# Optimization experiments

Hardware: AMD Instinct MI355X
Metric: run time of the kernel (lower is better)

## Reference

```python
import jax, jax.numpy as jnp
import numpy as np

NUM_EXPERTS = 16
IN_FEATURES = 2048
OUT_FEATURES = 2048
RANK = 128
ALPHA = 32.0
TOKENS = 32768  # total packed tokens, multiple of NUM_EXPERTS (pad_seq_to_mult guarantees this)


def setup_inputs() -> dict:
    key = jax.random.key(0)
    k1, k2, k3 = jax.random.split(key, 3)
    x = jax.random.normal(k1, (TOKENS, IN_FEATURES), dtype=jnp.float32)
    # linear_in per-expert weights (kaiming-style random for reference)
    lora_a = jax.random.normal(k2, (NUM_EXPERTS, IN_FEATURES, RANK), dtype=jnp.float32) * (1.0 / np.sqrt(IN_FEATURES))
    # linear_out per-expert weights (LoRA convention init is zeros; random here for nontrivial check)
    lora_b = jax.random.normal(k3, (NUM_EXPERTS, RANK, OUT_FEATURES), dtype=jnp.float32) * (1.0 / np.sqrt(RANK))
    return {"x": x, "lora_a": lora_a, "lora_b": lora_b}


def reference(x, lora_a, lora_b):
    # Tokens are packed per expert with uniform counts (padding to a multiple of
    # NUM_EXPERTS is handled upstream by pad_seq_to_mult). Grouped LoRA:
    #   out_e = (x_e @ A_e) @ B_e * (alpha / rank)
    E = lora_a.shape[0]
    T, H = x.shape
    xg = x.reshape(E, T // E, H)                      # [E, Te, H]
    low = jnp.einsum('eth,ehr->etr', xg, lora_a)      # grouped GEMM 1: [E, Te, r]
    # activation = identity (adapter default)
    out = jnp.einsum('etr,ero->eto', low, lora_b)     # grouped GEMM 2: [E, Te, O]
    scale = ALPHA / RANK
    return (out * scale).reshape(T, -1)               # [T, O]
```

## Files before the change

### kernel.cpp

```cpp
#include <hip/hip_runtime.h>
#include <hip/hip_bf16.h>
#include <stdint.h>

#define NEXP   16
#define TTOK   32768
#define HIN    2048
#define RNK    128
#define OOUT   2048
#define TE     (TTOK / NEXP)
#define LORA_SCALE 0.25f

typedef __bf16 bf16_t;
typedef bf16_t bf16x8 __attribute__((ext_vector_type(8)));
typedef bf16_t bf16x4 __attribute__((ext_vector_type(4)));
typedef float  f32x4  __attribute__((ext_vector_type(4)));

__global__ void transpose_cvt_kernel(const float* __restrict__ src,
                                     bf16_t* __restrict__ dst,
                                     int Rr, int Cc)
{
    __shared__ float tile[32][33];
    const int e  = blockIdx.z;
    const int c0 = blockIdx.x * 32;
    const int r0 = blockIdx.y * 32;
    const float* s = src + (size_t)e * Rr * Cc;
    bf16_t*      d = dst + (size_t)e * Rr * Cc;
    const int tx = threadIdx.x & 31;
    const int ty = threadIdx.x >> 5;
#pragma unroll
    for (int j = 0; j < 32; j += 8)
        tile[ty + j][tx] = s[(size_t)(r0 + ty + j) * Cc + (c0 + tx)];
    __syncthreads();
#pragma unroll
    for (int j = 0; j < 32; j += 8)
        d[(size_t)(c0 + ty + j) * Rr + (r0 + tx)] = (bf16_t)tile[tx][ty + j];
}

__global__ __launch_bounds__(512, 2)
void fused_lora(const float* __restrict__ X,
                const bf16_t* __restrict__ Atw,
                const bf16_t* __restrict__ Btw,
                float* __restrict__ Out)
{
    __shared__ __align__(16) char lds[98304];

    const int tid  = threadIdx.x;
    const int blk  = blockIdx.x;
    const int m0   = blk * 128;
    const int e    = blk >> 4;

    const int wave = tid >> 6;
    const int lane = tid & 63;
    const int lm   = lane & 15;
    const int q    = lane >> 4;
    const int wr   = (wave >> 1) * 32;
    const int wc   = (wave & 1) * 64;

    const int sr  = tid >> 2;
    const int sc  = tid & 3;
    const int ssw = (sr & 7) << 4;

    const float*  xg = X   + (size_t)(m0 + sr) * HIN + sc * 16;
    const bf16_t* ag = Atw + ((size_t)e * RNK + sr) * HIN + sc * 16;

    f32x4  xa[4];
    bf16x8 ar[2];
    f32x4  acc1[2][4] = {};

    {
#pragma unroll
        for (int i = 0; i < 4; ++i) xa[i] = *(const f32x4*)(xg + i * 4);
        ar[0] = *(const bf16x8*)(ag);
        ar[1] = *(const bf16x8*)(ag + 8);
        bf16x8 c0, c1;
#pragma unroll
        for (int i = 0; i < 4; ++i) {
            c0[i] = (bf16_t)xa[0][i]; c0[4 + i] = (bf16_t)xa[1][i];
            c1[i] = (bf16_t)xa[2][i]; c1[4 + i] = (bf16_t)xa[3][i];
        }
        char* bx = lds + sr * 128;
        *(bf16x8*)(bx + ((sc * 32     ) ^ ssw)) = c0;
        *(bf16x8*)(bx + ((sc * 32 + 16) ^ ssw)) = c1;
        char* ba = lds + 32768 + sr * 128;
        *(bf16x8*)(ba + ((sc * 32     ) ^ ssw)) = ar[0];
        *(bf16x8*)(ba + ((sc * 32 + 16) ^ ssw)) = ar[1];
    }
    __syncthreads();

    for (int it = 0; it < 32; ++it) {
        const int cur = it & 1;
        if (it < 31) {
            const float*  px = xg + (it + 1) * 64;
            const bf16_t* pa = ag + (it + 1) * 64;
#pragma unroll
            for (int i = 0; i < 4; ++i) xa[i] = *(const f32x4*)(px + i * 4);
            ar[0] = *(const bf16x8*)(pa);
            ar[1] = *(const bf16x8*)(pa + 8);
        }
        const char* xb = lds + cur * 16384;
        const char* ab = lds + 32768 + cur * 16384;
#pragma unroll
        for (int ks = 0; ks < 2; ++ks) {
            bf16x8 XF[2], AF[4];
#pragma unroll
            for (int mt = 0; mt < 2; ++mt) {
                const int row = wr + mt * 16 + lm;
                XF[mt] = *(const bf16x8*)(xb + row * 128 +
                           ((ks * 64 + q * 16) ^ ((row & 7) << 4)));
            }
#pragma unroll
            for (int rt = 0; rt < 4; ++rt) {
                const int row = wc + rt * 16 + lm;
                AF[rt] = *(const bf16x8*)(ab + row * 128 +
                           ((ks * 64 + q * 16) ^ ((row & 7) << 4)));
            }
#pragma unroll
            for (int mt = 0; mt < 2; ++mt)
#pragma unroll
                for (int rt = 0; rt < 4; ++rt)
                    acc1[mt][rt] = __builtin_amdgcn_mfma_f32_16x16x32_bf16(
                        AF[rt], XF[mt], acc1[mt][rt], 0, 0, 0);
        }
        if (it < 31) {
            bf16x8 c0, c1;
#pragma unroll
            for (int i = 0; i < 4; ++i) {
                c0[i] = (bf16_t)xa[0][i]; c0[4 + i] = (bf16_t)xa[1][i];
                c1[i] = (bf16_t)xa[2][i]; c1[4 + i] = (bf16_t)xa[3][i];
            }
            char* bx = lds + (cur ^ 1) * 16384 + sr * 128;
            *(bf16x8*)(bx + ((sc * 32     ) ^ ssw)) = c0;
            *(bf16x8*)(bx + ((sc * 32 + 16) ^ ssw)) = c1;
            char* ba = lds + 32768 + (cur ^ 1) * 16384 + sr * 128;
            *(bf16x8*)(ba + ((sc * 32     ) ^ ssw)) = ar[0];
            *(bf16x8*)(ba + ((sc * 32 + 16) ^ ssw)) = ar[1];
        }
        __syncthreads();
    }

    bf16x8 br[4];
    const bf16_t* bg0 = Btw + ((size_t)e * OOUT + sr) * RNK + sc * 32;
#pragma unroll
    for (int i = 0; i < 4; ++i) br[i] = *(const bf16x8*)(bg0 + i * 8);

    char* Lbase = lds + 65536;
#pragma unroll
    for (int mt = 0; mt < 2; ++mt) {
        const int m   = wr + mt * 16 + lm;
        const int msw = (m & 7) << 4;
#pragma unroll
        for (int rt = 0; rt < 4; ++rt) {
            const int r0 = wc + rt * 16 + q * 4;
            bf16x4 v;
#pragma unroll
            for (int i = 0; i < 4; ++i) v[i] = (bf16_t)acc1[mt][rt][i];
            *(bf16x4*)(Lbase + m * 256 + ((r0 * 2) ^ msw)) = v;
        }
    }
    __syncthreads();

    bf16x8 af2[2][4];
#pragma unroll
    for (int mt = 0; mt < 2; ++mt) {
        const int m   = wr + mt * 16 + lm;
        const int msw = (m & 7) << 4;
#pragma unroll
        for (int ks = 0; ks < 4; ++ks)
            af2[mt][ks] = *(const bf16x8*)(Lbase + m * 256 +
                             ((ks * 64 + q * 16) ^ msw));
    }

    {
        char* bb = lds + sr * 256;
#pragma unroll
        for (int i = 0; i < 4; ++i)
            *(bf16x8*)(bb + ((sc * 64 + i * 16) ^ ssw)) = br[i];
    }
    __syncthreads();

    for (int c = 0; c < 16; ++c) {
        const int cur = c & 1;
        if (c < 15) {
            const bf16_t* bg = bg0 + (size_t)(c + 1) * 128 * RNK;
#pragma unroll
            for (int i = 0; i < 4; ++i) br[i] = *(const bf16x8*)(bg + i * 8);
        }
        f32x4 acc2[2][4] = {};
        const char* bb = lds + cur * 32768;
#pragma unroll
        for (int nt = 0; nt < 4; ++nt) {
            const int n   = wc + nt * 16 + lm;
            const int nsw = (n & 7) << 4;
#pragma unroll
            for (int ks = 0; ks < 4; ++ks) {
                const bf16x8 bfr = *(const bf16x8*)(bb + n * 256 +
                                      ((ks * 64 + q * 16) ^ nsw));
                acc2[0][nt] = __builtin_amdgcn_mfma_f32_16x16x32_bf16(
                    bfr, af2[0][ks], acc2[0][nt], 0, 0, 0);
                acc2[1][nt] = __builtin_amdgcn_mfma_f32_16x16x32_bf16(
                    bfr, af2[1][ks], acc2[1][nt], 0, 0, 0);
            }
        }
#pragma unroll
        for (int mt = 0; mt < 2; ++mt) {
            const int gm = m0 + wr + mt * 16 + lm;
            float* orow = Out + (size_t)gm * OOUT + c * 128 + wc + q * 4;
#pragma unroll
            for (int nt = 0; nt < 4; ++nt) {
                const f32x4 v = acc2[mt][nt] * LORA_SCALE;
                *(f32x4*)(orow + nt * 16) = v;
            }
        }
        if (c < 15) {
            char* bb2 = lds + (cur ^ 1) * 32768 + sr * 256;
#pragma unroll
            for (int i = 0; i < 4; ++i)
                *(bf16x8*)(bb2 + ((sc * 64 + i * 16) ^ ssw)) = br[i];
        }
        __syncthreads();
    }
}

extern "C" void kernel_launch(void* const* d_in, const int* in_sizes, int n_in,
                              void* d_out, int out_size, void* d_ws, size_t ws_size,
                              hipStream_t stream)
{
    const float* x  = (const float*)d_in[0];
    const float* la = (const float*)d_in[1];
    const float* lb = (const float*)d_in[2];
    float* out = (float*)d_out;

    bf16_t* At  = (bf16_t*)d_ws;
    bf16_t* Btw = At + (size_t)NEXP * RNK * HIN;

    {
        dim3 g(RNK / 32, HIN / 32, NEXP);
        transpose_cvt_kernel<<<g, 256, 0, stream>>>(la, At, HIN, RNK);
    }
    {
        dim3 g(OOUT / 32, RNK / 32, NEXP);
        transpose_cvt_kernel<<<g, 256, 0, stream>>>(lb, Btw, RNK, OOUT);
    }
    fused_lora<<<dim3(TTOK / 128), dim3(512), 0, stream>>>(x, At, Btw, out);
}
```

Before: 526.7 us.

## Halve token tile to 64 rows and swizzle block order for more occupancy

Result: faster. 503.8 us (-4.3%).

```diff
diff --git a/kernel.cpp b/kernel.cpp
--- a/kernel.cpp
+++ b/kernel.cpp
@@ -7,7 +7,7 @@
 #define HIN    2048
 #define RNK    128
 #define OOUT   2048
-#define TE     (TTOK / NEXP)
+#define BM     64
 #define LORA_SCALE 0.25f
 
 typedef __bf16 bf16_t;
@@ -36,54 +36,49 @@
         d[(size_t)(c0 + ty + j) * Rr + (r0 + tx)] = (bf16_t)tile[tx][ty + j];
 }
 
-__global__ __launch_bounds__(512, 2)
+__global__ __launch_bounds__(512, 4)
 void fused_lora(const float* __restrict__ X,
                 const bf16_t* __restrict__ Atw,
                 const bf16_t* __restrict__ Btw,
                 float* __restrict__ Out)
 {
-    __shared__ __align__(16) char lds[98304];
-
-    const int tid  = threadIdx.x;
-    const int blk  = blockIdx.x;
-    const int m0   = blk * 128;
-    const int e    = blk >> 4;
+    __shared__ __align__(16) char lds[65536];
+
+    const int tid = threadIdx.x;
+    const int bid = blockIdx.x;
+    const int blk = (bid & 7) * 64 + (bid >> 3);
+    const int m0  = blk * BM;
+    const int e   = blk >> 5;
 
     const int wave = tid >> 6;
     const int lane = tid & 63;
     const int lm   = lane & 15;
     const int q    = lane >> 4;
-    const int wr   = (wave >> 1) * 32;
-    const int wc   = (wave & 1) * 64;
-
-    const int sr  = tid >> 2;
-    const int sc  = tid & 3;
-    const int ssw = (sr & 7) << 4;
-
-    const float*  xg = X   + (size_t)(m0 + sr) * HIN + sc * 16;
-    const bf16_t* ag = Atw + ((size_t)e * RNK + sr) * HIN + sc * 16;
-
-    f32x4  xa[4];
-    bf16x8 ar[2];
-    f32x4  acc1[2][4] = {};
-
-    {
-#pragma unroll
-        for (int i = 0; i < 4; ++i) xa[i] = *(const f32x4*)(xg + i * 4);
-        ar[0] = *(const bf16x8*)(ag);
-        ar[1] = *(const bf16x8*)(ag + 8);
-        bf16x8 c0, c1;
-#pragma unroll
-        for (int i = 0; i < 4; ++i) {
-            c0[i] = (bf16_t)xa[0][i]; c0[4 + i] = (bf16_t)xa[1][i];
-            c1[i] = (bf16_t)xa[2][i]; c1[4 + i] = (bf16_t)xa[3][i];
-        }
-        char* bx = lds + sr * 128;
-        *(bf16x8*)(bx + ((sc * 32     ) ^ ssw)) = c0;
-        *(bf16x8*)(bx + ((sc * 32 + 16) ^ ssw)) = c1;
-        char* ba = lds + 32768 + sr * 128;
-        *(bf16x8*)(ba + ((sc * 32     ) ^ ssw)) = ar[0];
-        *(bf16x8*)(ba + ((sc * 32 + 16) ^ ssw)) = ar[1];
+    const int wr   = (wave & 1) * 32;
+    const int wc   = (wave >> 1) * 32;
+
+    const int sxr = tid >> 3, sxc = tid & 7;
+    const int sar = tid >> 2, sac = tid & 3;
+
+    const float*  xg = X   + (size_t)(m0 + sxr) * HIN + sxc * 8;
+    const bf16_t* ag = Atw + ((size_t)e * RNK + sar) * HIN + sac * 16;
+
+    f32x4  xa0, xa1;
+    bf16x8 ar0, ar1;
+    f32x4  acc1[2][2] = {};
+
+    {
+        xa0 = *(const f32x4*)(xg);
+        xa1 = *(const f32x4*)(xg + 4);
+        ar0 = *(const bf16x8*)(ag);
+        ar1 = *(const bf16x8*)(ag + 8);
+        bf16x8 cx;
+#pragma unroll
+        for (int i = 0; i < 4; ++i) { cx[i] = (bf16_t)xa0[i]; cx[4 + i] = (bf16_t)xa1[i]; }
+        const int xsw = (sxr & 7) << 4, asw = (sar & 7) << 4;
+        *(bf16x8*)(lds + sxr * 128 + ((sxc * 16) ^ xsw)) = cx;
+        *(bf16x8*)(lds + 16384 + sar * 128 + ((sac * 32     ) ^ asw)) = ar0;
+        *(bf16x8*)(lds + 16384 + sar * 128 + ((sac * 32 + 16) ^ asw)) = ar1;
     }
     __syncthreads();
 
@@ -92,16 +87,16 @@
         if (it < 31) {
             const float*  px = xg + (it + 1) * 64;
             const bf16_t* pa = ag + (it + 1) * 64;
-#pragma unroll
-            for (int i = 0; i < 4; ++i) xa[i] = *(const f32x4*)(px + i * 4);
-            ar[0] = *(const bf16x8*)(pa);
-            ar[1] = *(const bf16x8*)(pa + 8);
-        }
-        const char* xb = lds + cur * 16384;
-        const char* ab = lds + 32768 + cur * 16384;
+            xa0 = *(const f32x4*)px;
+            xa1 = *(const f32x4*)(px + 4);
+            ar0 = *(const bf16x8*)pa;
+            ar1 = *(const bf16x8*)(pa + 8);
+        }
+        const char* xb = lds + cur * 8192;
+        const char* ab = lds + 16384 + cur * 16384;
 #pragma unroll
         for (int ks = 0; ks < 2; ++ks) {
-            bf16x8 XF[2], AF[4];
+            bf16x8 XF[2], AF[2];
 #pragma unroll
             for (int mt = 0; mt < 2; ++mt) {
                 const int row = wr + mt * 16 + lm;
@@ -109,52 +104,47 @@
                            ((ks * 64 + q * 16) ^ ((row & 7) << 4)));
             }
 #pragma unroll
-            for (int rt = 0; rt < 4; ++rt) {
-                const int row = wc + rt * 16 + lm;
-                AF[rt] = *(const bf16x8*)(ab + row * 128 +
+            for (int ct = 0; ct < 2; ++ct) {
+                const int row = wc + ct * 16 + lm;
+                AF[ct] = *(const bf16x8*)(ab + row * 128 +
                            ((ks * 64 + q * 16) ^ ((row & 7) << 4)));
             }
 #pragma unroll
             for (int mt = 0; mt < 2; ++mt)
 #pragma unroll
-                for (int rt = 0; rt < 4; ++rt)
-                    acc1[mt][rt] = __builtin_amdgcn_mfma_f32_16x16x32_bf16(
-                        AF[rt], XF[mt], acc1[mt][rt], 0, 0, 0);
+                for (int ct = 0; ct < 2; ++ct)
+                    acc1[mt][ct] = __builtin_amdgcn_mfma_f32_16x16x32_bf16(
+                        AF[ct], XF[mt], acc1[mt][ct], 0, 0, 0);
         }
         if (it < 31) {
-            bf16x8 c0, c1;
-#pragma unroll
-            for (int i = 0; i < 4; ++i) {
-                c0[i] = (bf16_t)xa[0][i]; c0[4 + i] = (bf16_t)xa[1][i];
-                c1[i] = (bf16_t)xa[2][i]; c1[4 + i] = (bf16_t)xa[3][i];
-            }
-            char* bx = lds + (cur ^ 1) * 16384 + sr * 128;
-            *(bf16x8*)(bx + ((sc * 32     ) ^ ssw)) = c0;
-            *(bf16x8*)(bx + ((sc * 32 + 16) ^ ssw)) = c1;
-            char* ba = lds + 32768 + (cur ^ 1) * 16384 + sr * 128;
-            *(bf16x8*)(ba + ((sc * 32     ) ^ ssw)) = ar[0];
-            *(bf16x8*)(ba + ((sc * 32 + 16) ^ ssw)) = ar[1];
+            bf16x8 cx;
+#pragma unroll
+            for (int i = 0; i < 4; ++i) { cx[i] = (bf16_t)xa0[i]; cx[4 + i] = (bf16_t)xa1[i]; }
+            const int xsw = (sxr & 7) << 4, asw = (sar & 7) << 4;
+            *(bf16x8*)(lds + (cur ^ 1) * 8192 + sxr * 128 + ((sxc * 16) ^ xsw)) = cx;
+            *(bf16x8*)(lds + 16384 + (cur ^ 1) * 16384 + sar * 128 + ((sac * 32     ) ^ asw)) = ar0;
+            *(bf16x8*)(lds + 16384 + (cur ^ 1) * 16384 + sar * 128 + ((sac * 32 + 16) ^ asw)) = ar1;
         }
         __syncthreads();
     }
 
     bf16x8 br[4];
-    const bf16_t* bg0 = Btw + ((size_t)e * OOUT + sr) * RNK + sc * 32;
+    const bf16_t* bg0 = Btw + ((size_t)e * OOUT + sar) * RNK + sac * 32;
 #pragma unroll
     for (int i = 0; i < 4; ++i) br[i] = *(const bf16x8*)(bg0 + i * 8);
 
-    char* Lbase = lds + 65536;
+    char* Lb = lds + 49152;
 #pragma unroll
     for (int mt = 0; mt < 2; ++mt) {
         const int m   = wr + mt * 16 + lm;
         const int msw = (m & 7) << 4;
 #pragma unroll
-        for (int rt = 0; rt < 4; ++rt) {
-            const int r0 = wc + rt * 16 + q * 4;
+        for (int ct = 0; ct < 2; ++ct) {
+            const int r0 = wc + ct * 16 + q * 4;
             bf16x4 v;
 #pragma unroll
-            for (int i = 0; i < 4; ++i) v[i] = (bf16_t)acc1[mt][rt][i];
-            *(bf16x4*)(Lbase + m * 256 + ((r0 * 2) ^ msw)) = v;
+            for (int i = 0; i < 4; ++i) v[i] = (bf16_t)acc1[mt][ct][i];
+            *(bf16x4*)(Lb + m * 256 + ((r0 * 2) ^ msw)) = v;
         }
     }
     __syncthreads();
@@ -166,15 +156,15 @@
         const int msw = (m & 7) << 4;
 #pragma unroll
         for (int ks = 0; ks < 4; ++ks)
-            af2[mt][ks] = *(const bf16x8*)(Lbase + m * 256 +
-                             ((ks * 64 + q * 16) ^ msw));
-    }
-
-    {
-        char* bb = lds + sr * 256;
+            af2[mt][ks] = *(const bf16x8*)(Lb + m * 256 + ((ks * 64 + q * 16) ^ msw));
+    }
+
+    {
+        char* bb = lds + sar * 256;
+        const int bsw = (sar & 7) << 4;
 #pragma unroll
         for (int i = 0; i < 4; ++i)
-            *(bf16x8*)(bb + ((sc * 64 + i * 16) ^ ssw)) = br[i];
+            *(bf16x8*)(bb + ((sac * 64 + i * 16) ^ bsw)) = br[i];
     }
     __syncthreads();
 
@@ -185,20 +175,20 @@
 #pragma unroll
             for (int i = 0; i < 4; ++i) br[i] = *(const bf16x8*)(bg + i * 8);
         }
-        f32x4 acc2[2][4] = {};
+        f32x4 acc2[2][2] = {};
         const char* bb = lds + cur * 32768;
 #pragma unroll
-        for (int nt = 0; nt < 4; ++nt) {
+        for (int nt = 0; nt < 2; ++nt) {
             const int n   = wc + nt * 16 + lm;
             const int nsw = (n & 7) << 4;
 #pragma unroll
             for (int ks = 0; ks < 4; ++ks) {
-                const bf16x8 bfr = *(const bf16x8*)(bb + n * 256 +
-                                      ((ks * 64 + q * 16) ^ nsw));
+                const bf16x8 BF = *(const bf16x8*)(bb + n * 256 +
+                                     ((ks * 64 + q * 16) ^ nsw));
                 acc2[0][nt] = __builtin_amdgcn_mfma_f32_16x16x32_bf16(
-                    bfr, af2[0][ks], acc2[0][nt], 0, 0, 0);
+                    BF, af2[0][ks], acc2[0][nt], 0, 0, 0);
                 acc2[1][nt] = __builtin_amdgcn_mfma_f32_16x16x32_bf16(
-                    bfr, af2[1][ks], acc2[1][nt], 0, 0, 0);
+                    BF, af2[1][ks], acc2[1][nt], 0, 0, 0);
             }
         }
 #pragma unroll
@@ -206,16 +196,17 @@
             const int gm = m0 + wr + mt * 16 + lm;
             float* orow = Out + (size_t)gm * OOUT + c * 128 + wc + q * 4;
 #pragma unroll
-            for (int nt = 0; nt < 4; ++nt) {
+            for (int nt = 0; nt < 2; ++nt) {
                 const f32x4 v = acc2[mt][nt] * LORA_SCALE;
                 *(f32x4*)(orow + nt * 16) = v;
             }
         }
         if (c < 15) {
-            char* bb2 = lds + (cur ^ 1) * 32768 + sr * 256;
+            char* bb2 = lds + (cur ^ 1) * 32768 + sar * 256;
+            const int bsw = (sar & 7) << 4;
 #pragma unroll
             for (int i = 0; i < 4; ++i)
-                *(bf16x8*)(bb2 + ((sc * 64 + i * 16) ^ ssw)) = br[i];
+                *(bf16x8*)(bb2 + ((sac * 64 + i * 16) ^ bsw)) = br[i];
         }
         __syncthreads();
     }
@@ -241,5 +232,5 @@
         dim3 g(OOUT / 32, RNK / 32, NEXP);
         transpose_cvt_kernel<<<g, 256, 0, stream>>>(lb, Btw, RNK, OOUT);
     }
-    fused_lora<<<dim3(TTOK / 128), dim3(512), 0, stream>>>(x, At, Btw, out);
+    fused_lora<<<dim3(TTOK / BM), dim3(512), 0, stream>>>(x, At, Btw, out);
 }
```
